# Kernel optimization log

Measured on AMD Instinct MI355X. Metric: run time of the kernel, lower is better.

## Reference

```python
import jax, jax.numpy as jnp
import numpy as np

T, B, INP = 64, 4, 768
Q = E = 384  # hidden // divisor = 1536 // 4
DFF = 2 * INP


def _binop(ei, ej):
    # masked associative operator for the linear recurrence s_t = f_t*s_{t-1}+c_t
    ui, xi, mi = ei
    uj, xj, mj = ej
    cond = mj > 0
    return (jnp.where(cond, uj, uj * ui),
            jnp.where(cond, xj, uj * xi + xj),
            jnp.where(cond, mj, mi))


def setup_inputs() -> dict:
    key = jax.random.key(0)
    ks = jax.random.split(key, 10)
    n = lambda i, shp: jax.random.normal(ks[i], shp, jnp.float32)
    inp = n(0, (T, B, INP))
    is_first = (jax.random.uniform(ks[1], (T, B, 1)) < 0.05).astype(jnp.float32)
    drops = jnp.ones((T, B, 1), jnp.float32)            # eval-mode dropout mask
    init_inp = jnp.zeros((B, INP), jnp.float32)
    init_state = jnp.zeros((B, Q * E), jnp.float32)
    return {
        'inp': inp, 'is_first': is_first, 'drops': drops,
        'init_inp': init_inp, 'init_state': init_state,
        'mix_mu': jax.random.uniform(ks[2], (INP,), jnp.float32),
        'mix_W': n(3, (INP, Q)) / np.sqrt(INP),
        'layer_W': n(4, (INP, 2 * Q + 2 * E)) / np.sqrt(INP),
        'proj_W': n(5, (E, INP)) / np.sqrt(E),
        'rms_w': jnp.ones((E,), jnp.float32),
        'ln_w': jnp.ones((INP,), jnp.float32),
        'ln_b': jnp.zeros((INP,), jnp.float32),
        'ffn_W1': n(6, (INP, DFF)) / np.sqrt(INP),
        'ffn_W2': n(7, (INP, DFF)) / np.sqrt(INP),
        'ffn_W3': n(8, (DFF, INP)) / np.sqrt(DFF),
    }


def reference(inp, is_first, drops, init_inp, init_state, mix_mu, mix_W,
              layer_W, proj_W, rms_w, ln_w, ln_b, ffn_W1, ffn_W2, ffn_W3):
    Tt, Bb, _ = inp.shape
    Qd, Ed = mix_W.shape[1], proj_W.shape[0]
    init = init_state.reshape(Bb, Qd, Ed)[None]                 # [1,B,Q,E]
    init_masks = jnp.concatenate([jnp.ones_like(is_first[:1]), is_first[1:]], 0)
    lasts = jnp.concatenate([jnp.zeros_like(inp[:1]), inp[:-1]], 0)
    lasts = lasts + init_masks * (init_inp[None] - lasts)
    # components
    mixed = mix_mu * inp + (1.0 - mix_mu) * lasts               # MixingLayer
    forget = jax.nn.sigmoid(mixed @ mix_W)                      # [T,B,Q]
    forget = (forget - 1.0) * drops + 1.0
    parts = (inp @ layer_W) * drops                             # [T,B,2Q+2E]
    qk = jax.nn.elu(parts[..., :2 * Qd]) + 1.0
    query, keyv = qk[..., :Qd], qk[..., Qd:]
    reset, value = parts[..., 2 * Qd:2 * Qd + Ed], parts[..., 2 * Qd + Ed:]
    value = jax.nn.sigmoid(reset) * value
    cand = keyv[..., :, None] * value[..., None, :]             # [T,B,Q,E]
    forget_b = jnp.broadcast_to(forget[..., None], cand.shape)
    cands = cand + init_masks[..., None] * forget_b * init
    masks = jnp.broadcast_to(is_first[..., None], cand.shape)
    # masked log-depth parallel scan of s_t = f_t*s_{t-1} + c_t
    states = jax.lax.associative_scan(_binop, (forget_b, cands, masks), axis=0)[1]
    out = jnp.einsum('tbq,tbqe->tbe', query, states)            # query @ state
    out = out * jax.lax.rsqrt(jnp.mean(out * out, -1, keepdims=True) + 1e-6) * rms_w
    out = out @ proj_W                                          # [T,B,INP]
    # RNNCell: residual + LayerNorm + gated FFN (SwiGLU-style GatingLayer)
    h = inp + out
    mu = jnp.mean(h, -1, keepdims=True)
    var = jnp.var(h, -1, keepdims=True)
    h = (h - mu) * jax.lax.rsqrt(var + 1e-5) * ln_w + ln_b
    return (jax.nn.silu(h @ ffn_W1) * (h @ ffn_W2)) @ ffn_W3
```

## Files before the change

kernel.cpp:

```cpp
#include <hip/hip_runtime.h>
#include <hip/hip_bf16.h>

#define T_DIM 64
#define B_DIM 4
#define INP_D 768
#define Q_D   384
#define E_D   384
#define DFF_D 1536
#define NTOK  256

typedef short bf16x8 __attribute__((ext_vector_type(8)));
typedef float f32x4  __attribute__((ext_vector_type(4)));

__device__ __forceinline__ float sigf(float x)  { return 1.0f / (1.0f + __expf(-x)); }
__device__ __forceinline__ float elu1f(float x) { return x > 0.0f ? x + 1.0f : __expf(x); }

__device__ __forceinline__ short f2b(float x) {
  union { __hip_bfloat16 b; short s; } u;
  u.b = __float2bfloat16(x);
  return u.s;
}
__device__ __forceinline__ bf16x8 cvt8(float4 a, float4 b) {
  bf16x8 r;
  r[0] = f2b(a.x); r[1] = f2b(a.y); r[2] = f2b(a.z); r[3] = f2b(a.w);
  r[4] = f2b(b.x); r[5] = f2b(b.y); r[6] = f2b(b.z); r[7] = f2b(b.w);
  return r;
}

#define WS_FORGET 0
#define WS_QUERY  98304
#define WS_KEYV   196608
#define WS_VALUE  294912
#define WS_PATT   393216
#define WS_ATTN   1179648
#define WS_HPRE   1277952
#define WS_H      1474560
#define WS_G      1671168
#define WS_BF     2064384
#define PK_MIX   0
#define PK_LAYER 294912
#define PK_PROJ  1474560
#define PK_W1    1769472
#define PK_W2    2949120
#define PK_W3    4128768

__global__ __launch_bounds__(256) void k_conv(const float* __restrict__ mixW,
                                              const float* __restrict__ layerW,
                                              const float* __restrict__ projW,
                                              const float* __restrict__ W1,
                                              const float* __restrict__ W2,
                                              const float* __restrict__ W3,
                                              short* __restrict__ wsb) {
  const int blk = blockIdx.x;
  const float* src; short* dst; int N, kb, nb64;
  if (blk < 144)        { src = mixW;   dst = wsb + PK_MIX;   N = 384;  int r = blk;        kb = r / 6;  nb64 = r % 6; }
  else if (blk < 720)   { src = layerW; dst = wsb + PK_LAYER; N = 1536; int r = blk - 144;  kb = r / 24; nb64 = r % 24; }
  else if (blk < 864)   { src = projW;  dst = wsb + PK_PROJ;  N = 768;  int r = blk - 720;  kb = r / 12; nb64 = r % 12; }
  else if (blk < 1440)  { src = W1;     dst = wsb + PK_W1;    N = 1536; int r = blk - 864;  kb = r / 24; nb64 = r % 24; }
  else if (blk < 2016)  { src = W2;     dst = wsb + PK_W2;    N = 1536; int r = blk - 1440; kb = r / 24; nb64 = r % 24; }
  else                  { src = W3;     dst = wsb + PK_W3;    N = 768;  int r = blk - 2016; kb = r / 12; nb64 = r % 12; }

  __shared__ float lds[32][68];
  const int tid = threadIdx.x;
  {
    const int r = tid >> 3, c8 = (tid & 7) * 8;
    const float* p = &src[(size_t)(kb * 32 + r) * N + nb64 * 64 + c8];
    *(float4*)&lds[r][c8]     = *(const float4*)p;
    *(float4*)&lds[r][c8 + 4] = *(const float4*)(p + 4);
  }
  __syncthreads();
  {
    const int nb = tid >> 6, lane = tid & 63, g = lane >> 4, c = lane & 15;
    unsigned int w[4];
#pragma unroll
    for (int jj = 0; jj < 4; ++jj) {
      unsigned short lo = (unsigned short)f2b(lds[g * 8 + jj * 2][nb * 16 + c]);
      unsigned short hi = (unsigned short)f2b(lds[g * 8 + jj * 2 + 1][nb * 16 + c]);
      w[jj] = (unsigned int)lo | ((unsigned int)hi << 16);
    }
    const int N16 = N >> 4;
    size_t o = ((size_t)kb * N16 + (nb64 * 4 + nb)) * 512 + lane * 8;
    uint4 pk; pk.x = w[0]; pk.y = w[1]; pk.z = w[2]; pk.w = w[3];
    *(uint4*)&dst[o] = pk;
  }
}

template<int KSTEPS, bool DUAL, class ALoad>
__device__ __forceinline__ void mm_core(ALoad loadA,
                                        const short* __restrict__ B1, int bn1, int N16a,
                                        const short* __restrict__ B2, int bn2, int N16b,
                                        int lane, f32x4* acc1, f32x4* acc2) {
  bf16x8 a_c = loadA(0);
  bf16x8 b1c[4], b2c[4];
#pragma unroll
  for (int s = 0; s < 4; ++s)
    b1c[s] = *(const bf16x8*)&B1[((size_t)(bn1 + s)) * 512 + lane * 8];
  if constexpr (DUAL) {
#pragma unroll
    for (int s = 0; s < 4; ++s)
      b2c[s] = *(const bf16x8*)&B2[((size_t)(bn2 + s)) * 512 + lane * 8];
  }
#pragma unroll 2
  for (int kb = 0; kb < KSTEPS; ++kb) {
    bf16x8 a_n = a_c;
    bf16x8 b1n[4], b2n[4];
    if (kb + 1 < KSTEPS) {
      a_n = loadA(kb + 1);
#pragma unroll
      for (int s = 0; s < 4; ++s)
        b1n[s] = *(const bf16x8*)&B1[((size_t)(kb + 1) * N16a + bn1 + s) * 512 + lane * 8];
      if constexpr (DUAL) {
#pragma unroll
        for (int s = 0; s < 4; ++s)
          b2n[s] = *(const bf16x8*)&B2[((size_t)(kb + 1) * N16b + bn2 + s) * 512 + lane * 8];
      }
    }
#pragma unroll
    for (int s = 0; s < 4; ++s)
      acc1[s] = __builtin_amdgcn_mfma_f32_16x16x32_bf16(a_c, b1c[s], acc1[s], 0, 0, 0);
    if constexpr (DUAL) {
#pragma unroll
      for (int s = 0; s < 4; ++s)
        acc2[s] = __builtin_amdgcn_mfma_f32_16x16x32_bf16(a_c, b2c[s], acc2[s], 0, 0, 0);
    }
    a_c = a_n;
#pragma unroll
    for (int s = 0; s < 4; ++s) b1c[s] = b1n[s];
    if constexpr (DUAL) {
#pragma unroll
      for (int s = 0; s < 4; ++s) b2c[s] = b2n[s];
    }
  }
}

#define WAVE_SETUP  const int tid = threadIdx.x, w = tid >> 6, l = tid & 63; \
                    const int m0 = blockIdx.x * 64; \
                    const int rowA = m0 + w * 16 + (l & 15); \
                    const int kg = (l >> 4) * 8; (void)kg;

__global__ __launch_bounds__(256) void k_fg(const float* __restrict__ inp,
                                            const float* __restrict__ is_first,
                                            const float* __restrict__ init_inp,
                                            const float* __restrict__ mu,
                                            const short* __restrict__ Bp,
                                            const float* __restrict__ drops,
                                            float* __restrict__ forget) {
  WAVE_SETUP
  const int n0 = blockIdx.y * 64, bn = blockIdx.y * 4;
  const int tt = rowA >> 2, bb = rowA & 3;
  const float fr = (tt == 0) ? 1.0f : is_first[rowA];
  const float* lastp = (fr > 0.5f) ? &init_inp[bb * INP_D] : &inp[(size_t)(rowA - 4) * INP_D];
  const float* inpp  = &inp[(size_t)rowA * INP_D];
  auto loadA = [&](int kb) -> bf16x8 {
    const int k = kb * 32 + kg;
    float4 x0 = *(const float4*)&inpp[k],  x1 = *(const float4*)&inpp[k + 4];
    float4 l0 = *(const float4*)&lastp[k], l1 = *(const float4*)&lastp[k + 4];
    float4 m0v = *(const float4*)&mu[k],   m1v = *(const float4*)&mu[k + 4];
    float4 r0, r1;
    r0.x = m0v.x * x0.x + (1.0f - m0v.x) * l0.x;
    r0.y = m0v.y * x0.y + (1.0f - m0v.y) * l0.y;
    r0.z = m0v.z * x0.z + (1.0f - m0v.z) * l0.z;
    r0.w = m0v.w * x0.w + (1.0f - m0v.w) * l0.w;
    r1.x = m1v.x * x1.x + (1.0f - m1v.x) * l1.x;
    r1.y = m1v.y * x1.y + (1.0f - m1v.y) * l1.y;
    r1.z = m1v.z * x1.z + (1.0f - m1v.z) * l1.z;
    r1.w = m1v.w * x1.w + (1.0f - m1v.w) * l1.w;
    return cvt8(r0, r1);
  };
  f32x4 acc[4];
#pragma unroll
  for (int s = 0; s < 4; ++s) acc[s] = (f32x4){0.f, 0.f, 0.f, 0.f};
  mm_core<24, false>(loadA, Bp, bn, 24, nullptr, 0, 0, l, acc, nullptr);
#pragma unroll
  for (int i = 0; i < 4; ++i) {
    const int row = m0 + w * 16 + ((l >> 4) << 2) + i;
    const float d = drops[row];
#pragma unroll
    for (int s = 0; s < 4; ++s) {
      const int col = n0 + s * 16 + (l & 15);
      forget[(size_t)row * Q_D + col] = (sigf(acc[s][i]) - 1.0f) * d + 1.0f;
    }
  }
}

__global__ __launch_bounds__(256) void k_parts(const float* __restrict__ inp,
                                               const short* __restrict__ Lp,
                                               const float* __restrict__ drops,
                                               float* __restrict__ query,
                                               float* __restrict__ keyv,
                                               float* __restrict__ value) {
  WAVE_SETUP
  const int jy = blockIdx.y;
  const float* Ap = &inp[(size_t)rowA * INP_D];
  auto loadA = [&](int kb) -> bf16x8 {
    const int k = kb * 32 + kg;
    return cvt8(*(const float4*)&Ap[k], *(const float4*)&Ap[k + 4]);
  };
  if (jy < 12) {
    float* dst = (jy < 6) ? query : keyv;
    const int nloc = ((jy < 6) ? jy : jy - 6) * 64;
    const int bn = jy * 4;
    f32x4 acc[4];
#pragma unroll
    for (int s = 0; s < 4; ++s) acc[s] = (f32x4){0.f, 0.f, 0.f, 0.f};
    mm_core<24, false>(loadA, Lp, bn, 96, nullptr, 0, 0, l, acc, nullptr);
#pragma unroll
    for (int i = 0; i < 4; ++i) {
      const int row = m0 + w * 16 + ((l >> 4) << 2) + i;
      const float d = drops[row];
#pragma unroll
      for (int s = 0; s < 4; ++s) {
        const int col = nloc + s * 16 + (l & 15);
        dst[(size_t)row * Q_D + col] = elu1f(acc[s][i] * d);
      }
    }
  } else {
    const int q = jy - 12;
    const int bn_r = 48 + q * 4, bn_v = 72 + q * 4;
    f32x4 a1[4], a2[4];
#pragma unroll
    for (int s = 0; s < 4; ++s) { a1[s] = (f32x4){0.f, 0.f, 0.f, 0.f}; a2[s] = (f32x4){0.f, 0.f, 0.f, 0.f}; }
    mm_core<24, true>(loadA, Lp, bn_r, 96, Lp, bn_v, 96, l, a1, a2);
#pragma unroll
    for (int i = 0; i < 4; ++i) {
      const int row = m0 + w * 16 + ((l >> 4) << 2) + i;
      const float d = drops[row];
#pragma unroll
      for (int s = 0; s < 4; ++s) {
        const int col = q * 64 + s * 16 + (l & 15);
        value[(size_t)row * E_D + col] = sigf(a1[s][i] * d) * (a2[s][i] * d);
      }
    }
  }
}

__global__ __launch_bounds__(256) void k_proj(const float* __restrict__ attn,
                                              const short* __restrict__ Bp,
                                              const float* __restrict__ inp,
                                              float* __restrict__ hpre) {
  WAVE_SETUP
  const int n0 = blockIdx.y * 64, bn = blockIdx.y * 4;
  const float* Ap = &attn[(size_t)rowA * E_D];
  auto loadA = [&](int kb) -> bf16x8 {
    const int k = kb * 32 + kg;
    return cvt8(*(const float4*)&Ap[k], *(const float4*)&Ap[k + 4]);
  };
  f32x4 acc[4];
#pragma unroll
  for (int s = 0; s < 4; ++s) acc[s] = (f32x4){0.f, 0.f, 0.f, 0.f};
  mm_core<12, false>(loadA, Bp, bn, 48, nullptr, 0, 0, l, acc, nullptr);
#pragma unroll
  for (int i = 0; i < 4; ++i) {
    const int row = m0 + w * 16 + ((l >> 4) << 2) + i;
#pragma unroll
    for (int s = 0; s < 4; ++s) {
      const int col = n0 + s * 16 + (l & 15);
      hpre[(size_t)row * INP_D + col] = acc[s][i] + inp[(size_t)row * INP_D + col];
    }
  }
}

__global__ __launch_bounds__(256) void k_ffn(const float* __restrict__ h,
                                             const short* __restrict__ W1p,
                                             const short* __restrict__ W2p,
                                             float* __restrict__ g) {
  WAVE_SETUP
  const int n0 = blockIdx.y * 64, bn = blockIdx.y * 4;
  const float* Ap = &h[(size_t)rowA * INP_D];
  auto loadA = [&](int kb) -> bf16x8 {
    const int k = kb * 32 + kg;
    return cvt8(*(const float4*)&Ap[k], *(const float4*)&Ap[k + 4]);
  };
  f32x4 a1[4], a2[4];
#pragma unroll
  for (int s = 0; s < 4; ++s) { a1[s] = (f32x4){0.f, 0.f, 0.f, 0.f}; a2[s] = (f32x4){0.f, 0.f, 0.f, 0.f}; }
  mm_core<24, true>(loadA, W1p, bn, 96, W2p, bn, 96, l, a1, a2);
#pragma unroll
  for (int i = 0; i < 4; ++i) {
    const int row = m0 + w * 16 + ((l >> 4) << 2) + i;
#pragma unroll
    for (int s = 0; s < 4; ++s) {
      const int col = n0 + s * 16 + (l & 15);
      const float v1 = a1[s][i], v2 = a2[s][i];
      g[(size_t)row * DFF_D + col] = v1 * sigf(v1) * v2;
    }
  }
}

__global__ __launch_bounds__(256) void k_out(const float* __restrict__ g,
                                             const short* __restrict__ Bp,
                                             float* __restrict__ out) {
  WAVE_SETUP
  const int n0 = blockIdx.y * 64, bn = blockIdx.y * 4;
  const float* Ap = &g[(size_t)rowA * DFF_D];
  auto loadA = [&](int kb) -> bf16x8 {
    const int k = kb * 32 + kg;
    return cvt8(*(const float4*)&Ap[k], *(const float4*)&Ap[k + 4]);
  };
  f32x4 acc[4];
#pragma unroll
  for (int s = 0; s < 4; ++s) acc[s] = (f32x4){0.f, 0.f, 0.f, 0.f};
  mm_core<48, false>(loadA, Bp, bn, 48, nullptr, 0, 0, l, acc, nullptr);
#pragma unroll
  for (int i = 0; i < 4; ++i) {
    const int row = m0 + w * 16 + ((l >> 4) << 2) + i;
#pragma unroll
    for (int s = 0; s < 4; ++s) {
      const int col = n0 + s * 16 + (l & 15);
      out[(size_t)row * INP_D + col] = acc[s][i];
    }
  }
}

__global__ __launch_bounds__(256) void k_scan(const float* __restrict__ forget,
                                              const float* __restrict__ query,
                                              const float* __restrict__ keyv,
                                              const float* __restrict__ value,
                                              const float* __restrict__ is_first,
                                              const float* __restrict__ init_state,
                                              float* __restrict__ patt) {
  __shared__ float stg[144];
  __shared__ float pacc[256];
  const int tid = threadIdx.x;
  const int e  = blockIdx.x * 64 + (tid & 63);
  const int qg = tid >> 6;
  const int qc = blockIdx.y;
  const int b  = blockIdx.z;
  const int q0 = qc * 48 + qg * 12;

  float s[12], ini[12];
#pragma unroll
  for (int j = 0; j < 12; ++j) {
    ini[j] = init_state[((size_t)b * Q_D + q0 + j) * E_D + e];
    s[j]   = ini[j];
  }

  float stage_r = 0.0f, v_r, if_r;
  {
    const int tok = b;
    if (tid < 144) {
      const int which = tid / 48, o = tid % 48;
      const float* src = which == 0 ? forget : (which == 1 ? keyv : query);
      stage_r = src[(size_t)tok * Q_D + qc * 48 + o];
    }
    v_r  = value[(size_t)tok * E_D + e];
    if_r = 0.0f;
  }

  for (int t = 0; t < T_DIM; ++t) {
    const int tok = t * B_DIM + b;
    if (tid < 144) stg[tid] = stage_r;
    const float v  = v_r;
    const float ff = if_r;
    __syncthreads();
    if (t + 1 < T_DIM) {
      const int tok1 = tok + B_DIM;
      if (tid < 144) {
        const int which = tid / 48, o = tid % 48;
        const float* src = which == 0 ? forget : (which == 1 ? keyv : query);
        stage_r = src[(size_t)tok1 * Q_D + qc * 48 + o];
      }
      v_r  = value[(size_t)tok1 * E_D + e];
      if_r = is_first[tok1];
    }
    if (ff > 0.5f) {
#pragma unroll
      for (int j = 0; j < 12; ++j) s[j] = ini[j];
    }
    const float4* f4 = (const float4*)&stg[qg * 12];
    const float4* k4 = (const float4*)&stg[48 + qg * 12];
    const float4* q4 = (const float4*)&stg[96 + qg * 12];
    float p = 0.0f;
#pragma unroll
    for (int jj = 0; jj < 3; ++jj) {
      const float4 fv = f4[jj], kv = k4[jj], qv = q4[jj];
#pragma unroll
      for (int j2 = 0; j2 < 4; ++j2) {
        const int sj = jj * 4 + j2;
        s[sj] = fmaf((&fv.x)[j2], s[sj], (&kv.x)[j2] * v);
        p     = fmaf((&qv.x)[j2], s[sj], p);
      }
    }
    pacc[tid] = p;
    __syncthreads();
    if (tid < 64) {
      float r = pacc[tid] + pacc[tid + 64] + pacc[tid + 128] + pacc[tid + 192];
      patt[((size_t)qc * NTOK + tok) * E_D + blockIdx.x * 64 + tid] = r;
    }
    __syncthreads();
  }
}

__global__ __launch_bounds__(128) void ep_rms(const float* __restrict__ patt,
                                              const float* __restrict__ rms_w,
                                              float* __restrict__ attn) {
  const int tok = blockIdx.x, tid = threadIdx.x;
  float x[3], ss = 0.0f;
#pragma unroll
  for (int i = 0; i < 3; ++i) {
    const int e = i * 128 + tid;
    float a = 0.0f;
#pragma unroll
    for (int qc = 0; qc < 8; ++qc) a += patt[((size_t)qc * NTOK + tok) * E_D + e];
    x[i] = a;
    ss = fmaf(a, a, ss);
  }
#pragma unroll
  for (int off = 32; off; off >>= 1) ss += __shfl_down(ss, off, 64);
  __shared__ float r[2];
  const int wid = tid >> 6, lane = tid & 63;
  if (lane == 0) r[wid] = ss;
  __syncthreads();
  ss = r[0] + r[1];
  const float sc = rsqrtf(ss * (1.0f / E_D) + 1e-6f);
#pragma unroll
  for (int i = 0; i < 3; ++i) {
    const int e = i * 128 + tid;
    attn[(size_t)tok * E_D + e] = x[i] * sc * rms_w[e];
  }
}

__global__ __launch_bounds__(256) void ep_ln(const float* __restrict__ hpre,
                                             const float* __restrict__ ln_w,
                                             const float* __restrict__ ln_b,
                                             float* __restrict__ h) {
  const int tok = blockIdx.x, tid = threadIdx.x;
  float x[3], s1 = 0.0f, s2 = 0.0f;
#pragma unroll
  for (int i = 0; i < 3; ++i) {
    x[i] = hpre[(size_t)tok * INP_D + i * 256 + tid];
    s1 += x[i];
    s2 = fmaf(x[i], x[i], s2);
  }
#pragma unroll
  for (int off = 32; off; off >>= 1) {
    s1 += __shfl_down(s1, off, 64);
    s2 += __shfl_down(s2, off, 64);
  }
  __shared__ float r1[4], r2[4];
  const int wid = tid >> 6, lane = tid & 63;
  if (lane == 0) { r1[wid] = s1; r2[wid] = s2; }
  __syncthreads();
  s1 = r1[0] + r1[1] + r1[2] + r1[3];
  s2 = r2[0] + r2[1] + r2[2] + r2[3];
  const float mean = s1 * (1.0f / INP_D);
  const float var  = s2 * (1.0f / INP_D) - mean * mean;
  const float sc   = rsqrtf(var + 1e-5f);
#pragma unroll
  for (int i = 0; i < 3; ++i) {
    const int c = i * 256 + tid;
    h[(size_t)tok * INP_D + c] = (x[i] - mean) * sc * ln_w[c] + ln_b[c];
  }
}

extern "C" void kernel_launch(void* const* d_in, const int* in_sizes, int n_in,
                              void* d_out, int out_size, void* d_ws, size_t ws_size,
                              hipStream_t stream) {
  (void)in_sizes; (void)n_in; (void)out_size; (void)ws_size;
  const float* inp        = (const float*)d_in[0];
  const float* is_first   = (const float*)d_in[1];
  const float* drops      = (const float*)d_in[2];
  const float* init_inp   = (const float*)d_in[3];
  const float* init_state = (const float*)d_in[4];
  const float* mix_mu     = (const float*)d_in[5];
  const float* mix_W      = (const float*)d_in[6];
  const float* layer_W    = (const float*)d_in[7];
  const float* proj_W     = (const float*)d_in[8];
  const float* rms_w      = (const float*)d_in[9];
  const float* ln_w       = (const float*)d_in[10];
  const float* ln_b       = (const float*)d_in[11];
  const float* W1         = (const float*)d_in[12];
  const float* W2         = (const float*)d_in[13];
  const float* W3         = (const float*)d_in[14];
  float* out = (float*)d_out;
  float* ws  = (float*)d_ws;
  short* wsb = (short*)(ws + WS_BF);

  float* forget = ws + WS_FORGET;
  float* query  = ws + WS_QUERY;
  float* keyv   = ws + WS_KEYV;
  float* value  = ws + WS_VALUE;
  float* patt   = ws + WS_PATT;
  float* attn   = ws + WS_ATTN;
  float* hpre   = ws + WS_HPRE;
  float* h      = ws + WS_H;
  float* g      = ws + WS_G;

  k_conv<<<2592, 256, 0, stream>>>(mix_W, layer_W, proj_W, W1, W2, W3, wsb);
  k_fg<<<dim3(4, 6), 256, 0, stream>>>(inp, is_first, init_inp, mix_mu,
                                       wsb + PK_MIX, drops, forget);
  k_parts<<<dim3(4, 18), 256, 0, stream>>>(inp, wsb + PK_LAYER, drops, query, keyv, value);
  k_scan<<<dim3(6, 8, 4), 256, 0, stream>>>(forget, query, keyv, value,
                                            is_first, init_state, patt);
  ep_rms<<<NTOK, 128, 0, stream>>>(patt, rms_w, attn);
  k_proj<<<dim3(4, 12), 256, 0, stream>>>(attn, wsb + PK_PROJ, inp, hpre);
  ep_ln<<<NTOK, 256, 0, stream>>>(hpre, ln_w, ln_b, h);
  k_ffn<<<dim3(4, 24), 256, 0, stream>>>(h, wsb + PK_W1, wsb + PK_W2, g);
  k_out<<<dim3(4, 12), 256, 0, stream>>>(g, wsb + PK_W3, out);
}
```

Before: 209.9 us.

## Halve GEMM N-tiles to double grid size and merge forget/parts kernels

Adds a SUBT template parameter to the MFMA core so each block computes 32 output columns instead of 64, doubling the block count for the proj, FFN and output GEMMs so more of the GPU's compute units are busy at this small token count. The separate forget-gate and q/k/value projection kernels are merged into one launch with 48 column tiles, removing a kernel launch and letting both run concurrently. The cost is that each A row tile is loaded and converted to bf16 twice as often, and each wave issues fewer MFMAs per load.

```diff
diff --git a/kernel.cpp b/kernel.cpp
--- a/kernel.cpp
+++ b/kernel.cpp
@@ -85,50 +85,50 @@
   }
 }
 
-template<int KSTEPS, bool DUAL, class ALoad>
+template<int KSTEPS, int SUBT, bool DUAL, class ALoad>
 __device__ __forceinline__ void mm_core(ALoad loadA,
                                         const short* __restrict__ B1, int bn1, int N16a,
                                         const short* __restrict__ B2, int bn2, int N16b,
                                         int lane, f32x4* acc1, f32x4* acc2) {
   bf16x8 a_c = loadA(0);
-  bf16x8 b1c[4], b2c[4];
-#pragma unroll
-  for (int s = 0; s < 4; ++s)
+  bf16x8 b1c[SUBT], b2c[SUBT];
+#pragma unroll
+  for (int s = 0; s < SUBT; ++s)
     b1c[s] = *(const bf16x8*)&B1[((size_t)(bn1 + s)) * 512 + lane * 8];
   if constexpr (DUAL) {
 #pragma unroll
-    for (int s = 0; s < 4; ++s)
+    for (int s = 0; s < SUBT; ++s)
       b2c[s] = *(const bf16x8*)&B2[((size_t)(bn2 + s)) * 512 + lane * 8];
   }
 #pragma unroll 2
   for (int kb = 0; kb < KSTEPS; ++kb) {
     bf16x8 a_n = a_c;
-    bf16x8 b1n[4], b2n[4];
+    bf16x8 b1n[SUBT], b2n[SUBT];
     if (kb + 1 < KSTEPS) {
       a_n = loadA(kb + 1);
 #pragma unroll
-      for (int s = 0; s < 4; ++s)
+      for (int s = 0; s < SUBT; ++s)
         b1n[s] = *(const bf16x8*)&B1[((size_t)(kb + 1) * N16a + bn1 + s) * 512 + lane * 8];
       if constexpr (DUAL) {
 #pragma unroll
-        for (int s = 0; s < 4; ++s)
+        for (int s = 0; s < SUBT; ++s)
           b2n[s] = *(const bf16x8*)&B2[((size_t)(kb + 1) * N16b + bn2 + s) * 512 + lane * 8];
       }
     }
 #pragma unroll
-    for (int s = 0; s < 4; ++s)
+    for (int s = 0; s < SUBT; ++s)
       acc1[s] = __builtin_amdgcn_mfma_f32_16x16x32_bf16(a_c, b1c[s], acc1[s], 0, 0, 0);
     if constexpr (DUAL) {
 #pragma unroll
-      for (int s = 0; s < 4; ++s)
+      for (int s = 0; s < SUBT; ++s)
         acc2[s] = __builtin_amdgcn_mfma_f32_16x16x32_bf16(a_c, b2c[s], acc2[s], 0, 0, 0);
     }
     a_c = a_n;
 #pragma unroll
-    for (int s = 0; s < 4; ++s) b1c[s] = b1n[s];
+    for (int s = 0; s < SUBT; ++s) b1c[s] = b1n[s];
     if constexpr (DUAL) {
 #pragma unroll
-      for (int s = 0; s < 4; ++s) b2c[s] = b2n[s];
+      for (int s = 0; s < SUBT; ++s) b2c[s] = b2n[s];
     }
   }
 }
@@ -138,96 +138,90 @@
                     const int rowA = m0 + w * 16 + (l & 15); \
                     const int kg = (l >> 4) * 8; (void)kg;
 
-__global__ __launch_bounds__(256) void k_fg(const float* __restrict__ inp,
-                                            const float* __restrict__ is_first,
-                                            const float* __restrict__ init_inp,
-                                            const float* __restrict__ mu,
-                                            const short* __restrict__ Bp,
-                                            const float* __restrict__ drops,
-                                            float* __restrict__ forget) {
-  WAVE_SETUP
-  const int n0 = blockIdx.y * 64, bn = blockIdx.y * 4;
-  const int tt = rowA >> 2, bb = rowA & 3;
-  const float fr = (tt == 0) ? 1.0f : is_first[rowA];
-  const float* lastp = (fr > 0.5f) ? &init_inp[bb * INP_D] : &inp[(size_t)(rowA - 4) * INP_D];
-  const float* inpp  = &inp[(size_t)rowA * INP_D];
-  auto loadA = [&](int kb) -> bf16x8 {
-    const int k = kb * 32 + kg;
-    float4 x0 = *(const float4*)&inpp[k],  x1 = *(const float4*)&inpp[k + 4];
-    float4 l0 = *(const float4*)&lastp[k], l1 = *(const float4*)&lastp[k + 4];
-    float4 m0v = *(const float4*)&mu[k],   m1v = *(const float4*)&mu[k + 4];
-    float4 r0, r1;
-    r0.x = m0v.x * x0.x + (1.0f - m0v.x) * l0.x;
-    r0.y = m0v.y * x0.y + (1.0f - m0v.y) * l0.y;
-    r0.z = m0v.z * x0.z + (1.0f - m0v.z) * l0.z;
-    r0.w = m0v.w * x0.w + (1.0f - m0v.w) * l0.w;
-    r1.x = m1v.x * x1.x + (1.0f - m1v.x) * l1.x;
-    r1.y = m1v.y * x1.y + (1.0f - m1v.y) * l1.y;
-    r1.z = m1v.z * x1.z + (1.0f - m1v.z) * l1.z;
-    r1.w = m1v.w * x1.w + (1.0f - m1v.w) * l1.w;
-    return cvt8(r0, r1);
-  };
-  f32x4 acc[4];
-#pragma unroll
-  for (int s = 0; s < 4; ++s) acc[s] = (f32x4){0.f, 0.f, 0.f, 0.f};
-  mm_core<24, false>(loadA, Bp, bn, 24, nullptr, 0, 0, l, acc, nullptr);
-#pragma unroll
-  for (int i = 0; i < 4; ++i) {
-    const int row = m0 + w * 16 + ((l >> 4) << 2) + i;
-    const float d = drops[row];
-#pragma unroll
-    for (int s = 0; s < 4; ++s) {
-      const int col = n0 + s * 16 + (l & 15);
-      forget[(size_t)row * Q_D + col] = (sigf(acc[s][i]) - 1.0f) * d + 1.0f;
-    }
-  }
-}
-
-__global__ __launch_bounds__(256) void k_parts(const float* __restrict__ inp,
+__global__ __launch_bounds__(256) void k_qkvfg(const float* __restrict__ inp,
+                                               const float* __restrict__ is_first,
+                                               const float* __restrict__ init_inp,
+                                               const float* __restrict__ mu,
+                                               const short* __restrict__ Mixp,
                                                const short* __restrict__ Lp,
                                                const float* __restrict__ drops,
+                                               float* __restrict__ forget,
                                                float* __restrict__ query,
                                                float* __restrict__ keyv,
                                                float* __restrict__ value) {
   WAVE_SETUP
-  const int jy = blockIdx.y;
+  const int y = blockIdx.y;
+  if (y < 12) {
+    const int n0 = y * 32, bn = y * 2;
+    const int tt = rowA >> 2, bb = rowA & 3;
+    const float fr = (tt == 0) ? 1.0f : is_first[rowA];
+    const float* lastp = (fr > 0.5f) ? &init_inp[bb * INP_D] : &inp[(size_t)(rowA - 4) * INP_D];
+    const float* inpp  = &inp[(size_t)rowA * INP_D];
+    auto loadA = [&](int kb) -> bf16x8 {
+      const int k = kb * 32 + kg;
+      float4 x0 = *(const float4*)&inpp[k],  x1 = *(const float4*)&inpp[k + 4];
+      float4 l0 = *(const float4*)&lastp[k], l1 = *(const float4*)&lastp[k + 4];
+      float4 m0v = *(const float4*)&mu[k],   m1v = *(const float4*)&mu[k + 4];
+      float4 r0, r1;
+      r0.x = m0v.x * x0.x + (1.0f - m0v.x) * l0.x;
+      r0.y = m0v.y * x0.y + (1.0f - m0v.y) * l0.y;
+      r0.z = m0v.z * x0.z + (1.0f - m0v.z) * l0.z;
+      r0.w = m0v.w * x0.w + (1.0f - m0v.w) * l0.w;
+      r1.x = m1v.x * x1.x + (1.0f - m1v.x) * l1.x;
+      r1.y = m1v.y * x1.y + (1.0f - m1v.y) * l1.y;
+      r1.z = m1v.z * x1.z + (1.0f - m1v.z) * l1.z;
+      r1.w = m1v.w * x1.w + (1.0f - m1v.w) * l1.w;
+      return cvt8(r0, r1);
+    };
+    f32x4 acc[2] = {(f32x4){0.f,0.f,0.f,0.f}, (f32x4){0.f,0.f,0.f,0.f}};
+    mm_core<24, 2, false>(loadA, Mixp, bn, 24, nullptr, 0, 0, l, acc, nullptr);
+#pragma unroll
+    for (int i = 0; i < 4; ++i) {
+      const int row = m0 + w * 16 + ((l >> 4) << 2) + i;
+      const float d = drops[row];
+#pragma unroll
+      for (int s = 0; s < 2; ++s) {
+        const int col = n0 + s * 16 + (l & 15);
+        forget[(size_t)row * Q_D + col] = (sigf(acc[s][i]) - 1.0f) * d + 1.0f;
+      }
+    }
+    return;
+  }
   const float* Ap = &inp[(size_t)rowA * INP_D];
   auto loadA = [&](int kb) -> bf16x8 {
     const int k = kb * 32 + kg;
     return cvt8(*(const float4*)&Ap[k], *(const float4*)&Ap[k + 4]);
   };
-  if (jy < 12) {
-    float* dst = (jy < 6) ? query : keyv;
-    const int nloc = ((jy < 6) ? jy : jy - 6) * 64;
-    const int bn = jy * 4;
-    f32x4 acc[4];
-#pragma unroll
-    for (int s = 0; s < 4; ++s) acc[s] = (f32x4){0.f, 0.f, 0.f, 0.f};
-    mm_core<24, false>(loadA, Lp, bn, 96, nullptr, 0, 0, l, acc, nullptr);
+  if (y < 36) {
+    const bool isq = (y < 24);
+    const int yy = isq ? y - 12 : y - 24;
+    float* dst = isq ? query : keyv;
+    const int bn = (isq ? 0 : 24) + yy * 2;
+    f32x4 acc[2] = {(f32x4){0.f,0.f,0.f,0.f}, (f32x4){0.f,0.f,0.f,0.f}};
+    mm_core<24, 2, false>(loadA, Lp, bn, 96, nullptr, 0, 0, l, acc, nullptr);
 #pragma unroll
     for (int i = 0; i < 4; ++i) {
       const int row = m0 + w * 16 + ((l >> 4) << 2) + i;
       const float d = drops[row];
 #pragma unroll
-      for (int s = 0; s < 4; ++s) {
-        const int col = nloc + s * 16 + (l & 15);
+      for (int s = 0; s < 2; ++s) {
+        const int col = yy * 32 + s * 16 + (l & 15);
         dst[(size_t)row * Q_D + col] = elu1f(acc[s][i] * d);
       }
     }
   } else {
-    const int q = jy - 12;
-    const int bn_r = 48 + q * 4, bn_v = 72 + q * 4;
-    f32x4 a1[4], a2[4];
-#pragma unroll
-    for (int s = 0; s < 4; ++s) { a1[s] = (f32x4){0.f, 0.f, 0.f, 0.f}; a2[s] = (f32x4){0.f, 0.f, 0.f, 0.f}; }
-    mm_core<24, true>(loadA, Lp, bn_r, 96, Lp, bn_v, 96, l, a1, a2);
+    const int q = y - 36;
+    const int bn_r = 48 + q * 2, bn_v = 72 + q * 2;
+    f32x4 a1[2] = {(f32x4){0.f,0.f,0.f,0.f}, (f32x4){0.f,0.f,0.f,0.f}};
+    f32x4 a2[2] = {(f32x4){0.f,0.f,0.f,0.f}, (f32x4){0.f,0.f,0.f,0.f}};
+    mm_core<24, 2, true>(loadA, Lp, bn_r, 96, Lp, bn_v, 96, l, a1, a2);
 #pragma unroll
     for (int i = 0; i < 4; ++i) {
       const int row = m0 + w * 16 + ((l >> 4) << 2) + i;
       const float d = drops[row];
 #pragma unroll
-      for (int s = 0; s < 4; ++s) {
-        const int col = q * 64 + s * 16 + (l & 15);
+      for (int s = 0; s < 2; ++s) {
+        const int col = q * 32 + s * 16 + (l & 15);
         value[(size_t)row * E_D + col] = sigf(a1[s][i] * d) * (a2[s][i] * d);
       }
     }
@@ -239,21 +233,19 @@
                                               const float* __restrict__ inp,
                                               float* __restrict__ hpre) {
   WAVE_SETUP
-  const int n0 = blockIdx.y * 64, bn = blockIdx.y * 4;
+  const int n0 = blockIdx.y * 32, bn = blockIdx.y * 2;
   const float* Ap = &attn[(size_t)rowA * E_D];
   auto loadA = [&](int kb) -> bf16x8 {
     const int k = kb * 32 + kg;
     return cvt8(*(const float4*)&Ap[k], *(const float4*)&Ap[k + 4]);
   };
-  f32x4 acc[4];
-#pragma unroll
-  for (int s = 0; s < 4; ++s) acc[s] = (f32x4){0.f, 0.f, 0.f, 0.f};
-  mm_core<12, false>(loadA, Bp, bn, 48, nullptr, 0, 0, l, acc, nullptr);
+  f32x4 acc[2] = {(f32x4){0.f,0.f,0.f,0.f}, (f32x4){0.f,0.f,0.f,0.f}};
+  mm_core<12, 2, false>(loadA, Bp, bn, 48, nullptr, 0, 0, l, acc, nullptr);
 #pragma unroll
   for (int i = 0; i < 4; ++i) {
     const int row = m0 + w * 16 + ((l >> 4) << 2) + i;
 #pragma unroll
-    for (int s = 0; s < 4; ++s) {
+    for (int s = 0; s < 2; ++s) {
       const int col = n0 + s * 16 + (l & 15);
       hpre[(size_t)row * INP_D + col] = acc[s][i] + inp[(size_t)row * INP_D + col];
     }
@@ -265,21 +257,20 @@
                                              const short* __restrict__ W2p,
                                              float* __restrict__ g) {
   WAVE_SETUP
-  const int n0 = blockIdx.y * 64, bn = blockIdx.y * 4;
+  const int n0 = blockIdx.y * 32, bn = blockIdx.y * 2;
   const float* Ap = &h[(size_t)rowA * INP_D];
   auto loadA = [&](int kb) -> bf16x8 {
     const int k = kb * 32 + kg;
     return cvt8(*(const float4*)&Ap[k], *(const float4*)&Ap[k + 4]);
   };
-  f32x4 a1[4], a2[4];
-#pragma unroll
-  for (int s = 0; s < 4; ++s) { a1[s] = (f32x4){0.f, 0.f, 0.f, 0.f}; a2[s] = (f32x4){0.f, 0.f, 0.f, 0.f}; }
-  mm_core<24, true>(loadA, W1p, bn, 96, W2p, bn, 96, l, a1, a2);
+  f32x4 a1[2] = {(f32x4){0.f,0.f,0.f,0.f}, (f32x4){0.f,0.f,0.f,0.f}};
+  f32x4 a2[2] = {(f32x4){0.f,0.f,0.f,0.f}, (f32x4){0.f,0.f,0.f,0.f}};
+  mm_core<24, 2, true>(loadA, W1p, bn, 96, W2p, bn, 96, l, a1, a2);
 #pragma unroll
   for (int i = 0; i < 4; ++i) {
     const int row = m0 + w * 16 + ((l >> 4) << 2) + i;
 #pragma unroll
-    for (int s = 0; s < 4; ++s) {
+    for (int s = 0; s < 2; ++s) {
       const int col = n0 + s * 16 + (l & 15);
       const float v1 = a1[s][i], v2 = a2[s][i];
       g[(size_t)row * DFF_D + col] = v1 * sigf(v1) * v2;
@@ -291,21 +282,19 @@
                                              const short* __restrict__ Bp,
                                              float* __restrict__ out) {
   WAVE_SETUP
-  const int n0 = blockIdx.y * 64, bn = blockIdx.y * 4;
+  const int n0 = blockIdx.y * 32, bn = blockIdx.y * 2;
   const float* Ap = &g[(size_t)rowA * DFF_D];
   auto loadA = [&](int kb) -> bf16x8 {
     const int k = kb * 32 + kg;
     return cvt8(*(const float4*)&Ap[k], *(const float4*)&Ap[k + 4]);
   };
-  f32x4 acc[4];
-#pragma unroll
-  for (int s = 0; s < 4; ++s) acc[s] = (f32x4){0.f, 0.f, 0.f, 0.f};
-  mm_core<48, false>(loadA, Bp, bn, 48, nullptr, 0, 0, l, acc, nullptr);
+  f32x4 acc[2] = {(f32x4){0.f,0.f,0.f,0.f}, (f32x4){0.f,0.f,0.f,0.f}};
+  mm_core<48, 2, false>(loadA, Bp, bn, 48, nullptr, 0, 0, l, acc, nullptr);
 #pragma unroll
   for (int i = 0; i < 4; ++i) {
     const int row = m0 + w * 16 + ((l >> 4) << 2) + i;
 #pragma unroll
-    for (int s = 0; s < 4; ++s) {
+    for (int s = 0; s < 2; ++s) {
       const int col = n0 + s * 16 + (l & 15);
       out[(size_t)row * INP_D + col] = acc[s][i];
     }
@@ -487,14 +476,14 @@
   float* g      = ws + WS_G;
 
   k_conv<<<2592, 256, 0, stream>>>(mix_W, layer_W, proj_W, W1, W2, W3, wsb);
-  k_fg<<<dim3(4, 6), 256, 0, stream>>>(inp, is_first, init_inp, mix_mu,
-                                       wsb + PK_MIX, drops, forget);
-  k_parts<<<dim3(4, 18), 256, 0, stream>>>(inp, wsb + PK_LAYER, drops, query, keyv, value);
+  k_qkvfg<<<dim3(4, 48), 256, 0, stream>>>(inp, is_first, init_inp, mix_mu,
+                                           wsb + PK_MIX, wsb + PK_LAYER, drops,
+                                           forget, query, keyv, value);
   k_scan<<<dim3(6, 8, 4), 256, 0, stream>>>(forget, query, keyv, value,
                                             is_first, init_state, patt);
   ep_rms<<<NTOK, 128, 0, stream>>>(patt, rms_w, attn);
-  k_proj<<<dim3(4, 12), 256, 0, stream>>>(attn, wsb + PK_PROJ, inp, hpre);
+  k_proj<<<dim3(4, 24), 256, 0, stream>>>(attn, wsb + PK_PROJ, inp, hpre);
   ep_ln<<<NTOK, 256, 0, stream>>>(hpre, ln_w, ln_b, h);
-  k_ffn<<<dim3(4, 24), 256, 0, stream>>>(h, wsb + PK_W1, wsb + PK_W2, g);
-  k_out<<<dim3(4, 12), 256, 0, stream>>>(g, wsb + PK_W3, out);
-}
+  k_ffn<<<dim3(4, 48), 256, 0, stream>>>(h, wsb + PK_W1, wsb + PK_W2, g);
+  k_out<<<dim3(4, 24), 256, 0, stream>>>(g, wsb + PK_W3, out);
+}
```

Measured after the change: 194.4 us. -7.4%, faster.
